# Performance work log

Measured on AMD Instinct MI355X. Metric: run time of the kernel, lower is better.

## Reference

```python
import jax, jax.numpy as jnp
import numpy as np

B, S, D = 4, 1024, 2048
H = 4096
NE = 8
TOPK = 2


def setup_inputs() -> dict:
    key = jax.random.key(0)
    ks = jax.random.split(key, 9)
    s = lambda fan_in: 1.0 / np.sqrt(fan_in)
    return {
        "x": jax.random.normal(ks[0], (B, S, D), dtype=jnp.float32),
        "W1": jax.random.normal(ks[1], (NE, D, H), dtype=jnp.float32) * s(D),
        "b1": jnp.zeros((NE, H), dtype=jnp.float32),
        "W2": jax.random.normal(ks[2], (NE, H, H), dtype=jnp.float32) * s(H),
        "b2": jnp.zeros((NE, H), dtype=jnp.float32),
        "W3": jax.random.normal(ks[3], (NE, H, D), dtype=jnp.float32) * s(H),
        "b3": jnp.zeros((NE, D), dtype=jnp.float32),
        "Wg": jax.random.normal(ks[4], (D, NE), dtype=jnp.float32) * s(D),
        "bg": jnp.zeros((NE,), dtype=jnp.float32),
    }


def reference(x, W1, b1, W2, b2, W3, b3, Wg, bg):
    # Gating: softmax over experts, then top-k
    gate_logits = jnp.einsum("bsd,dn->bsn", x, Wg) + bg          # [B,S,NE]
    gate_weights = jax.nn.softmax(gate_logits, axis=-1)
    topv, topi = jax.lax.top_k(gate_weights, TOPK)               # [B,S,K]

    # Dense compute of ALL experts (faithful to original)
    h = jax.nn.gelu(jnp.einsum("bsd,ndh->nbsh", x, W1) + b1[:, None, None, :], approximate=False)
    h = jax.nn.gelu(jnp.einsum("nbsh,nhf->nbsf", h, W2) + b2[:, None, None, :], approximate=False)
    eo = jnp.einsum("nbsf,nfd->nbsd", h, W3) + b3[:, None, None, :]  # [NE,B,S,D]

    # Weighted combine of top-k experts per token via sparse one-hot weights
    comb = jnp.sum(jax.nn.one_hot(topi, NE, dtype=x.dtype) * topv[..., None], axis=-2)  # [B,S,NE]
    out = jnp.einsum("nbsd,bsn->bsd", eo, comb)
    return out
```

## Files before the change

kernel.cpp:

```cpp
#include <hip/hip_runtime.h>
#include <math.h>

#define NT 4096
#define Dm 2048
#define Hm 4096
#define NEx 8
#define CAPROWS 9216

typedef float f32x4 __attribute__((ext_vector_type(4)));
typedef _Float16 f16x8 __attribute__((ext_vector_type(8)));

__global__ void k_init(int* meta) {
    if (threadIdx.x < NEx) meta[threadIdx.x] = 0;
}

__device__ __forceinline__ void conv_tile(const float* __restrict__ src, _Float16* __restrict__ dst,
                                          int K, int N, int t, float (*tile)[65]) {
    int nx = N >> 6, nk = K >> 6;
    int nb = t % nx;
    int kb = (t / nx) % nk;
    int e  = t / (nx * nk);
    int n0 = nb * 64, k0 = kb * 64;
    size_t ebase = (size_t)e * (size_t)K * (size_t)N;
    const float* S = src + ebase;
    _Float16* Dd = dst + ebase;
    int tx = threadIdx.x & 15, ty = threadIdx.x >> 4;
#pragma unroll
    for (int p = 0; p < 4; ++p) {
        int kr = p * 16 + ty;
        f32x4 v = *(const f32x4*)(S + (size_t)(k0 + kr) * N + n0 + tx * 4);
        tile[kr][tx * 4 + 0] = v[0]; tile[kr][tx * 4 + 1] = v[1];
        tile[kr][tx * 4 + 2] = v[2]; tile[kr][tx * 4 + 3] = v[3];
    }
    __syncthreads();
    int n = threadIdx.x >> 2, seg = threadIdx.x & 3;
    f16x8 o0, o1;
#pragma unroll
    for (int j = 0; j < 8; ++j) o0[j] = (_Float16)tile[seg * 16 + j][n];
#pragma unroll
    for (int j = 0; j < 8; ++j) o1[j] = (_Float16)tile[seg * 16 + 8 + j][n];
    _Float16* dp = Dd + (size_t)(n0 + n) * K + k0 + seg * 16;
    *(f16x8*)dp = o0;
    *(f16x8*)(dp + 8) = o1;
}

__global__ __launch_bounds__(256, 2) void k_convw(const float* __restrict__ src,
                                                  _Float16* __restrict__ dst, int K, int N) {
    __shared__ float tile[64][65];
    conv_tile(src, dst, K, N, blockIdx.x, tile);
}

__global__ __launch_bounds__(256, 2)
void k_gateconv(const float* __restrict__ x, const float* __restrict__ Wg,
                const float* __restrict__ bg, int* __restrict__ meta,
                int* __restrict__ list, float* __restrict__ topw,
                const float* __restrict__ csrc, _Float16* __restrict__ cdst,
                int cK, int cN) {
    __shared__ float tile[64][65];
    const int bid = blockIdx.x;
    if (bid >= NT / 4) {
        conv_tile(csrc, cdst, cK, cN, bid - NT / 4, tile);
        return;
    }
    int lane = threadIdx.x & 63;
    int t = bid * 4 + (threadIdx.x >> 6);
    const float* xr = x + (size_t)t * Dm;
    double acc[NEx];
#pragma unroll
    for (int j = 0; j < NEx; ++j) acc[j] = 0.0;
    for (int d = lane; d < Dm; d += 64) {
        double xv = (double)xr[d];
        const float* wr = Wg + (size_t)d * NEx;
#pragma unroll
        for (int j = 0; j < NEx; ++j) acc[j] += xv * (double)wr[j];
    }
#pragma unroll
    for (int off = 32; off > 0; off >>= 1) {
#pragma unroll
        for (int j = 0; j < NEx; ++j) acc[j] += __shfl_xor(acc[j], off, 64);
    }
    if (lane == 0) {
        double l[NEx];
#pragma unroll
        for (int j = 0; j < NEx; ++j) l[j] = acc[j] + (double)bg[j];
        double m = l[0];
        for (int j = 1; j < NEx; ++j) m = l[j] > m ? l[j] : m;
        double s = 0.0, ev[NEx];
        for (int j = 0; j < NEx; ++j) { ev[j] = exp(l[j] - m); s += ev[j]; }
        int i0 = 0; double v0 = l[0];
        for (int j = 1; j < NEx; ++j) if (l[j] > v0) { v0 = l[j]; i0 = j; }
        int i1 = -1; double v1 = -1e300;
        for (int j = 0; j < NEx; ++j) if (j != i0 && l[j] > v1) { v1 = l[j]; i1 = j; }
        topw[2 * t]     = (float)(ev[i0] / s);
        topw[2 * t + 1] = (float)(ev[i1] / s);
        int p0 = atomicAdd(&meta[i0], 1); list[i0 * NT + p0] = 2 * t;
        int p1 = atomicAdd(&meta[i1], 1); list[i1 * NT + p1] = 2 * t + 1;
    }
}

__global__ void k_plan(int* meta) {
    if (threadIdx.x == 0 && blockIdx.x == 0) {
        int tot = 0;
        for (int e = 0; e < NEx; ++e) {
            int c = meta[e];
            meta[8 + e] = c;
            int cp = (c + 127) & ~127;
            meta[16 + e] = cp;
            meta[24 + e] = tot;
            tot += cp;
        }
        meta[32] = tot;
    }
}

__global__ void k_gather(const float* __restrict__ x, const int* __restrict__ meta,
                         const int* __restrict__ list, int* __restrict__ pos_of,
                         _Float16* __restrict__ Xg) {
    int r = blockIdx.x;
    if (r >= meta[32]) return;
    int e = 0;
    while (r >= meta[24 + e + 1]) ++e;
    int i = r - meta[24 + e];
    _Float16* dst = Xg + (size_t)r * Dm + threadIdx.x * 8;
    if (i < meta[8 + e]) {
        int v = list[e * NT + i];
        int t = v >> 1;
        if (threadIdx.x == 0) pos_of[v] = r;
        const float* src = x + (size_t)t * Dm + threadIdx.x * 8;
        f32x4 a = *(const f32x4*)(src);
        f32x4 b = *(const f32x4*)(src + 4);
        f16x8 o;
        o[0] = (_Float16)a[0]; o[1] = (_Float16)a[1]; o[2] = (_Float16)a[2]; o[3] = (_Float16)a[3];
        o[4] = (_Float16)b[0]; o[5] = (_Float16)b[1]; o[6] = (_Float16)b[2]; o[7] = (_Float16)b[3];
        *(f16x8*)dst = o;
    } else {
        f16x8 z = (f16x8)(_Float16)0.0f;
        *(f16x8*)dst = z;
    }
}

__device__ __forceinline__ void gload16(const void* g, void* l) {
    __builtin_amdgcn_global_load_lds((__attribute__((address_space(1))) void*)(g),
                                     (__attribute__((address_space(3))) void*)(l),
                                     16, 0, 0);
}

__device__ __forceinline__ float gelu_f(float v) {
    return 0.5f * v * (1.0f + erff(v * 0.70710678118654752f));
}

template <int KDIM, int NDIM, bool GELU>
__global__ __launch_bounds__(256, 4)
void k_gemmconv(const _Float16* __restrict__ Abase, const _Float16* __restrict__ Wt,
                const float* __restrict__ bias, void* __restrict__ Cout,
                const int* __restrict__ meta,
                const float* __restrict__ csrc, _Float16* __restrict__ cdst,
                int cK, int cN, int nGemm) {
    __shared__ char smem[32768];
    const int bid = blockIdx.x;
    if (bid >= nGemm) {
        conv_tile(csrc, cdst, cK, cN, bid - nGemm, (float(*)[65])smem);
        return;
    }

    constexpr int GX = NDIM / 128;
    constexpr int GY = 32;
    constexpr int NBLK = GX * GY;
    const int e = bid / NBLK;
    const int f = bid % NBLK;
    const int fp = (f & 7) * (NBLK >> 3) + (f >> 3);
    const int nt = fp / GY;
    const int mt = fp % GY;
    const int cp = meta[16 + e];
    if (mt * 128 >= cp) return;
    const int row0 = meta[24 + e] + mt * 128;

    _Float16* ldsA = (_Float16*)smem;
    _Float16* ldsB = (_Float16*)(smem + 16384);

    const int tid = threadIdx.x;
    const int lane = tid & 63;
    const int wv = tid >> 6;
    const int wm = wv >> 1, wn = wv & 1;

    const char* Ag = (const char*)(Abase + (size_t)row0 * KDIM);
    const char* Bg = (const char*)(Wt + ((size_t)e * NDIM + (size_t)nt * 128) * KDIM);

    int soff[4];
#pragma unroll
    for (int r = 0; r < 4; ++r) {
        int L = r * 4096 + tid * 16;
        int row = L >> 7;
        int col = L & 127;
        int scol = col ^ ((row & 7) << 4);
        soff[r] = row * (KDIM * 2) + scol;
    }

    f32x4 acc[4][4];
#pragma unroll
    for (int i = 0; i < 4; ++i)
#pragma unroll
        for (int j = 0; j < 4; ++j)
            acc[i][j] = (f32x4){0.f, 0.f, 0.f, 0.f};

    int abase[4], aswz[4], bbase[4], bswz[4];
#pragma unroll
    for (int m = 0; m < 4; ++m) {
        int rA = wm * 64 + m * 16 + (lane & 15);
        abase[m] = rA * 128;
        aswz[m] = (rA & 7) << 4;
    }
#pragma unroll
    for (int n = 0; n < 4; ++n) {
        int rB = wn * 64 + n * 16 + (lane & 15);
        bbase[n] = rB * 128;
        bswz[n] = (rB & 7) << 4;
    }
    const int hib = (lane >> 4) * 16;

    const char* cldsA = (const char*)ldsA;
    const char* cldsB = (const char*)ldsB;

    for (int kt = 0; kt < KDIM / 64; ++kt) {
        const int kbyte = kt * 128;
#pragma unroll
        for (int r = 0; r < 4; ++r) {
            gload16(Ag + (soff[r] + kbyte), (char*)ldsA + r * 4096 + tid * 16);
            gload16(Bg + (soff[r] + kbyte), (char*)ldsB + r * 4096 + tid * 16);
        }
        __syncthreads();
#pragma unroll
        for (int ks = 0; ks < 2; ++ks) {
            const int cbs = ks * 64 + hib;
            f16x8 av[4], bv[4];
#pragma unroll
            for (int m = 0; m < 4; ++m)
                av[m] = *(const f16x8*)(cldsA + abase[m] + (cbs ^ aswz[m]));
#pragma unroll
            for (int n = 0; n < 4; ++n)
                bv[n] = *(const f16x8*)(cldsB + bbase[n] + (cbs ^ bswz[n]));
#pragma unroll
            for (int m = 0; m < 4; ++m)
#pragma unroll
                for (int n = 0; n < 4; ++n)
                    acc[m][n] = __builtin_amdgcn_mfma_f32_16x16x32_f16(av[m], bv[n], acc[m][n], 0, 0, 0);
        }
        __syncthreads();
    }

    const int lcol = lane & 15;
    const int rowq = (lane >> 4) * 4;
#pragma unroll
    for (int m = 0; m < 4; ++m) {
#pragma unroll
        for (int n = 0; n < 4; ++n) {
            const int gcol = nt * 128 + wn * 64 + n * 16 + lcol;
            const float bb = bias[(size_t)e * NDIM + gcol];
#pragma unroll
            for (int v = 0; v < 4; ++v) {
                const int grow = row0 + wm * 64 + m * 16 + rowq + v;
                float val = acc[m][n][v] + bb;
                if constexpr (GELU) {
                    ((_Float16*)Cout)[(size_t)grow * NDIM + gcol] = (_Float16)gelu_f(val);
                } else {
                    ((float*)Cout)[(size_t)grow * NDIM + gcol] = val;
                }
            }
        }
    }
}

__global__ void k_combine(const float* __restrict__ eo, const int* __restrict__ pos_of,
                          const float* __restrict__ topw, float* __restrict__ out) {
    int t = blockIdx.x;
    int r0 = pos_of[2 * t], r1 = pos_of[2 * t + 1];
    float w0 = topw[2 * t], w1 = topw[2 * t + 1];
    const f32x4* e0 = (const f32x4*)(eo + (size_t)r0 * Dm);
    const f32x4* e1 = (const f32x4*)(eo + (size_t)r1 * Dm);
    f32x4* op = (f32x4*)(out + (size_t)t * Dm);
    for (int i = threadIdx.x; i < Dm / 4; i += 256) {
        f32x4 a = e0[i], b = e1[i];
        op[i] = a * w0 + b * w1;
    }
}

extern "C" void kernel_launch(void* const* d_in, const int* in_sizes, int n_in,
                              void* d_out, int out_size, void* d_ws, size_t ws_size,
                              hipStream_t stream) {
    const float* x  = (const float*)d_in[0];
    const float* W1 = (const float*)d_in[1];
    const float* b1 = (const float*)d_in[2];
    const float* W2 = (const float*)d_in[3];
    const float* b2 = (const float*)d_in[4];
    const float* W3 = (const float*)d_in[5];
    const float* b3 = (const float*)d_in[6];
    const float* Wg = (const float*)d_in[7];
    const float* bg = (const float*)d_in[8];
    float* out = (float*)d_out;
    (void)in_sizes; (void)n_in; (void)out_size;

    char* ws = (char*)d_ws;
    int*   meta   = (int*)ws;
    int*   list   = (int*)(ws + 256);
    int*   pos_of = (int*)(ws + 256 + 131072);
    float* topw   = (float*)(ws + 256 + 131072 + 32768);
    size_t off = 196864;

    const int nC1 = (Hm / 64) * (Dm / 64) * NEx;
    const int nC2 = (Hm / 64) * (Hm / 64) * NEx;
    const int nC3 = (Dm / 64) * (Hm / 64) * NEx;
    const int nG12 = NEx * (Hm / 128) * 32;
    const int nG3  = NEx * (Dm / 128) * 32;

    const size_t sXg  = (size_t)CAPROWS * Dm * 2;
    const size_t sWb1 = (size_t)NEx * Dm * Hm * 2;
    const size_t sWb2 = (size_t)NEx * Hm * Hm * 2;
    const size_t sWb3 = (size_t)NEx * Hm * Dm * 2;
    const size_t sH   = (size_t)CAPROWS * Hm * 2;

    const size_t needPar = off + sXg + sWb1 + sWb2 + sWb3 + sH + sH;

    if (ws_size >= needPar) {
        _Float16* Xg  = (_Float16*)(ws + off); off += sXg;
        _Float16* Wb1 = (_Float16*)(ws + off); off += sWb1;
        _Float16* Wb2 = (_Float16*)(ws + off); off += sWb2;
        _Float16* Wb3 = (_Float16*)(ws + off); off += sWb3;
        _Float16* h1  = (_Float16*)(ws + off); off += sH;
        _Float16* h2  = (_Float16*)(ws + off); off += sH;
        float*    eo  = (float*)Wb1;

        k_init<<<1, 64, 0, stream>>>(meta);
        k_gateconv<<<NT / 4 + nC1, 256, 0, stream>>>(x, Wg, bg, meta, list, topw,
                                                     W1, Wb1, Dm, Hm);
        k_plan<<<1, 1, 0, stream>>>(meta);
        k_gather<<<CAPROWS, 256, 0, stream>>>(x, meta, list, pos_of, Xg);

        k_gemmconv<Dm, Hm, true><<<nG12 + nC2, 256, 0, stream>>>(
            Xg, Wb1, b1, (void*)h1, meta, W2, Wb2, Hm, Hm, nG12);
        k_gemmconv<Hm, Hm, true><<<nG12 + nC3, 256, 0, stream>>>(
            h1, Wb2, b2, (void*)h2, meta, W3, Wb3, Hm, Dm, nG12);
        k_gemmconv<Hm, Dm, false><<<nG3, 256, 0, stream>>>(
            h2, Wb3, b3, (void*)eo, meta, (const float*)0, (_Float16*)0, 0, 0, nG3);

        k_combine<<<NT, 256, 0, stream>>>(eo, pos_of, topw, out);
    } else {
        _Float16* Xg = (_Float16*)(ws + off); off += sXg;
        _Float16* Wb = (_Float16*)(ws + off); off += sWb2;
        _Float16* h2 = (_Float16*)(ws + off); off += sH;
        _Float16* h1 = (_Float16*)(ws + off);
        float*    eo = (float*)(ws + off);

        k_init<<<1, 64, 0, stream>>>(meta);
        k_gateconv<<<NT / 4, 256, 0, stream>>>(x, Wg, bg, meta, list, topw,
                                               (const float*)0, (_Float16*)0, 0, 0);
        k_plan<<<1, 1, 0, stream>>>(meta);
        k_gather<<<CAPROWS, 256, 0, stream>>>(x, meta, list, pos_of, Xg);

        k_convw<<<nC1, 256, 0, stream>>>(W1, Wb, Dm, Hm);
        k_gemmconv<Dm, Hm, true><<<nG12, 256, 0, stream>>>(
            Xg, Wb, b1, (void*)h1, meta, (const float*)0, (_Float16*)0, 0, 0, nG12);

        k_convw<<<nC2, 256, 0, stream>>>(W2, Wb, Hm, Hm);
        k_gemmconv<Hm, Hm, true><<<nG12, 256, 0, stream>>>(
            h1, Wb, b2, (void*)h2, meta, (const float*)0, (_Float16*)0, 0, 0, nG12);

        k_convw<<<nC3, 256, 0, stream>>>(W3, Wb, Hm, Dm);
        k_gemmconv<Hm, Dm, false><<<nG3, 256, 0, stream>>>(
            h2, Wb, b3, (void*)eo, meta, (const float*)0, (_Float16*)0, 0, 0, nG3);

        k_combine<<<NT, 256, 0, stream>>>(eo, pos_of, topw, out);
    }
}
```

Measured before the change: 1.098 ms.

## Fuse top-k combine into final expert GEMM epilogue via atomic adds

The final expert GEMM now scales each output row by its gate weight and atomically accumulates it into the output token row, using per-row token and weight tables written during gather. This removes the separate combine kernel and the fp32 expert-output round trip through memory. A memset of the output is added. The weight conversion tiles also switch to nontemporal loads and stores so streamed weights pollute the cache less. Atomic float adds make the summation order nondeterministic and add atomic traffic.

```diff
diff --git a/kernel.cpp b/kernel.cpp
--- a/kernel.cpp
+++ b/kernel.cpp
@@ -28,7 +28,7 @@
 #pragma unroll
     for (int p = 0; p < 4; ++p) {
         int kr = p * 16 + ty;
-        f32x4 v = *(const f32x4*)(S + (size_t)(k0 + kr) * N + n0 + tx * 4);
+        f32x4 v = __builtin_nontemporal_load((const f32x4*)(S + (size_t)(k0 + kr) * N + n0 + tx * 4));
         tile[kr][tx * 4 + 0] = v[0]; tile[kr][tx * 4 + 1] = v[1];
         tile[kr][tx * 4 + 2] = v[2]; tile[kr][tx * 4 + 3] = v[3];
     }
@@ -40,8 +40,8 @@
 #pragma unroll
     for (int j = 0; j < 8; ++j) o1[j] = (_Float16)tile[seg * 16 + 8 + j][n];
     _Float16* dp = Dd + (size_t)(n0 + n) * K + k0 + seg * 16;
-    *(f16x8*)dp = o0;
-    *(f16x8*)(dp + 8) = o1;
+    __builtin_nontemporal_store(o0, (f16x8*)dp);
+    __builtin_nontemporal_store(o1, (f16x8*)(dp + 8));
 }
 
 __global__ __launch_bounds__(256, 2) void k_convw(const float* __restrict__ src,
@@ -114,7 +114,8 @@
 }
 
 __global__ void k_gather(const float* __restrict__ x, const int* __restrict__ meta,
-                         const int* __restrict__ list, int* __restrict__ pos_of,
+                         const int* __restrict__ list, const float* __restrict__ topw,
+                         int* __restrict__ tok_of, float* __restrict__ wsc,
                          _Float16* __restrict__ Xg) {
     int r = blockIdx.x;
     if (r >= meta[32]) return;
@@ -125,7 +126,7 @@
     if (i < meta[8 + e]) {
         int v = list[e * NT + i];
         int t = v >> 1;
-        if (threadIdx.x == 0) pos_of[v] = r;
+        if (threadIdx.x == 0) { tok_of[r] = t; wsc[r] = topw[v]; }
         const float* src = x + (size_t)t * Dm + threadIdx.x * 8;
         f32x4 a = *(const f32x4*)(src);
         f32x4 b = *(const f32x4*)(src + 4);
@@ -134,6 +135,7 @@
         o[4] = (_Float16)b[0]; o[5] = (_Float16)b[1]; o[6] = (_Float16)b[2]; o[7] = (_Float16)b[3];
         *(f16x8*)dst = o;
     } else {
+        if (threadIdx.x == 0) { tok_of[r] = -1; wsc[r] = 0.0f; }
         f16x8 z = (f16x8)(_Float16)0.0f;
         *(f16x8*)dst = z;
     }
@@ -149,11 +151,13 @@
     return 0.5f * v * (1.0f + erff(v * 0.70710678118654752f));
 }
 
-template <int KDIM, int NDIM, bool GELU>
+template <int KDIM, int NDIM, bool GELU, bool FC>
 __global__ __launch_bounds__(256, 4)
 void k_gemmconv(const _Float16* __restrict__ Abase, const _Float16* __restrict__ Wt,
                 const float* __restrict__ bias, void* __restrict__ Cout,
                 const int* __restrict__ meta,
+                const int* __restrict__ tok_of, const float* __restrict__ wsc,
+                float* __restrict__ outp,
                 const float* __restrict__ csrc, _Float16* __restrict__ cdst,
                 int cK, int cN, int nGemm) {
     __shared__ char smem[32768];
@@ -250,37 +254,47 @@
 
     const int lcol = lane & 15;
     const int rowq = (lane >> 4) * 4;
-#pragma unroll
-    for (int m = 0; m < 4; ++m) {
-#pragma unroll
-        for (int n = 0; n < 4; ++n) {
-            const int gcol = nt * 128 + wn * 64 + n * 16 + lcol;
-            const float bb = bias[(size_t)e * NDIM + gcol];
+    if constexpr (FC) {
+        float bb[4];
+#pragma unroll
+        for (int n = 0; n < 4; ++n)
+            bb[n] = bias[(size_t)e * NDIM + nt * 128 + wn * 64 + n * 16 + lcol];
+#pragma unroll
+        for (int m = 0; m < 4; ++m) {
 #pragma unroll
             for (int v = 0; v < 4; ++v) {
                 const int grow = row0 + wm * 64 + m * 16 + rowq + v;
-                float val = acc[m][n][v] + bb;
-                if constexpr (GELU) {
-                    ((_Float16*)Cout)[(size_t)grow * NDIM + gcol] = (_Float16)gelu_f(val);
-                } else {
-                    ((float*)Cout)[(size_t)grow * NDIM + gcol] = val;
+                const int tok = tok_of[grow];
+                if (tok >= 0) {
+                    const float w = wsc[grow];
+                    float* orow = outp + (size_t)tok * NDIM;
+#pragma unroll
+                    for (int n = 0; n < 4; ++n) {
+                        const int gcol = nt * 128 + wn * 64 + n * 16 + lcol;
+                        atomicAdd(orow + gcol, w * (acc[m][n][v] + bb[n]));
+                    }
                 }
             }
         }
-    }
-}
-
-__global__ void k_combine(const float* __restrict__ eo, const int* __restrict__ pos_of,
-                          const float* __restrict__ topw, float* __restrict__ out) {
-    int t = blockIdx.x;
-    int r0 = pos_of[2 * t], r1 = pos_of[2 * t + 1];
-    float w0 = topw[2 * t], w1 = topw[2 * t + 1];
-    const f32x4* e0 = (const f32x4*)(eo + (size_t)r0 * Dm);
-    const f32x4* e1 = (const f32x4*)(eo + (size_t)r1 * Dm);
-    f32x4* op = (f32x4*)(out + (size_t)t * Dm);
-    for (int i = threadIdx.x; i < Dm / 4; i += 256) {
-        f32x4 a = e0[i], b = e1[i];
-        op[i] = a * w0 + b * w1;
+    } else {
+#pragma unroll
+        for (int m = 0; m < 4; ++m) {
+#pragma unroll
+            for (int n = 0; n < 4; ++n) {
+                const int gcol = nt * 128 + wn * 64 + n * 16 + lcol;
+                const float bb = bias[(size_t)e * NDIM + gcol];
+#pragma unroll
+                for (int v = 0; v < 4; ++v) {
+                    const int grow = row0 + wm * 64 + m * 16 + rowq + v;
+                    float val = acc[m][n][v] + bb;
+                    if constexpr (GELU) {
+                        ((_Float16*)Cout)[(size_t)grow * NDIM + gcol] = (_Float16)gelu_f(val);
+                    } else {
+                        ((float*)Cout)[(size_t)grow * NDIM + gcol] = val;
+                    }
+                }
+            }
+        }
     }
 }
 
@@ -297,14 +311,15 @@
     const float* Wg = (const float*)d_in[7];
     const float* bg = (const float*)d_in[8];
     float* out = (float*)d_out;
-    (void)in_sizes; (void)n_in; (void)out_size;
+    (void)in_sizes; (void)n_in;
 
     char* ws = (char*)d_ws;
     int*   meta   = (int*)ws;
     int*   list   = (int*)(ws + 256);
-    int*   pos_of = (int*)(ws + 256 + 131072);
-    float* topw   = (float*)(ws + 256 + 131072 + 32768);
-    size_t off = 196864;
+    int*   tok_of = (int*)(ws + 256 + 131072);
+    float* wsc    = (float*)(ws + 256 + 131072 + 36864);
+    float* topw   = (float*)(ws + 256 + 131072 + 73728);
+    size_t off = 237824;
 
     const int nC1 = (Hm / 64) * (Dm / 64) * NEx;
     const int nC2 = (Hm / 64) * (Hm / 64) * NEx;
@@ -319,6 +334,8 @@
     const size_t sH   = (size_t)CAPROWS * Hm * 2;
 
     const size_t needPar = off + sXg + sWb1 + sWb2 + sWb3 + sH + sH;
+
+    hipMemsetAsync(out, 0, (size_t)out_size * sizeof(float), stream);
 
     if (ws_size >= needPar) {
         _Float16* Xg  = (_Float16*)(ws + off); off += sXg;
@@ -327,47 +344,47 @@
         _Float16* Wb3 = (_Float16*)(ws + off); off += sWb3;
         _Float16* h1  = (_Float16*)(ws + off); off += sH;
         _Float16* h2  = (_Float16*)(ws + off); off += sH;
-        float*    eo  = (float*)Wb1;
 
         k_init<<<1, 64, 0, stream>>>(meta);
         k_gateconv<<<NT / 4 + nC1, 256, 0, stream>>>(x, Wg, bg, meta, list, topw,
                                                      W1, Wb1, Dm, Hm);
         k_plan<<<1, 1, 0, stream>>>(meta);
-        k_gather<<<CAPROWS, 256, 0, stream>>>(x, meta, list, pos_of, Xg);
-
-        k_gemmconv<Dm, Hm, true><<<nG12 + nC2, 256, 0, stream>>>(
-            Xg, Wb1, b1, (void*)h1, meta, W2, Wb2, Hm, Hm, nG12);
-        k_gemmconv<Hm, Hm, true><<<nG12 + nC3, 256, 0, stream>>>(
-            h1, Wb2, b2, (void*)h2, meta, W3, Wb3, Hm, Dm, nG12);
-        k_gemmconv<Hm, Dm, false><<<nG3, 256, 0, stream>>>(
-            h2, Wb3, b3, (void*)eo, meta, (const float*)0, (_Float16*)0, 0, 0, nG3);
-
-        k_combine<<<NT, 256, 0, stream>>>(eo, pos_of, topw, out);
+        k_gather<<<CAPROWS, 256, 0, stream>>>(x, meta, list, topw, tok_of, wsc, Xg);
+
+        k_gemmconv<Dm, Hm, true, false><<<nG12 + nC2, 256, 0, stream>>>(
+            Xg, Wb1, b1, (void*)h1, meta, (const int*)0, (const float*)0, (float*)0,
+            W2, Wb2, Hm, Hm, nG12);
+        k_gemmconv<Hm, Hm, true, false><<<nG12 + nC3, 256, 0, stream>>>(
+            h1, Wb2, b2, (void*)h2, meta, (const int*)0, (const float*)0, (float*)0,
+            W3, Wb3, Hm, Dm, nG12);
+        k_gemmconv<Hm, Dm, false, true><<<nG3, 256, 0, stream>>>(
+            h2, Wb3, b3, (void*)0, meta, tok_of, wsc, out,
+            (const float*)0, (_Float16*)0, 0, 0, nG3);
     } else {
         _Float16* Xg = (_Float16*)(ws + off); off += sXg;
         _Float16* Wb = (_Float16*)(ws + off); off += sWb2;
         _Float16* h2 = (_Float16*)(ws + off); off += sH;
         _Float16* h1 = (_Float16*)(ws + off);
-        float*    eo = (float*)(ws + off);
 
         k_init<<<1, 64, 0, stream>>>(meta);
         k_gateconv<<<NT / 4, 256, 0, stream>>>(x, Wg, bg, meta, list, topw,
                                                (const float*)0, (_Float16*)0, 0, 0);
         k_plan<<<1, 1, 0, stream>>>(meta);
-        k_gather<<<CAPROWS, 256, 0, stream>>>(x, meta, list, pos_of, Xg);
+        k_gather<<<CAPROWS, 256, 0, stream>>>(x, meta, list, topw, tok_of, wsc, Xg);
 
         k_convw<<<nC1, 256, 0, stream>>>(W1, Wb, Dm, Hm);
-        k_gemmconv<Dm, Hm, true><<<nG12, 256, 0, stream>>>(
-            Xg, Wb, b1, (void*)h1, meta, (const float*)0, (_Float16*)0, 0, 0, nG12);
+        k_gemmconv<Dm, Hm, true, false><<<nG12, 256, 0, stream>>>(
+            Xg, Wb, b1, (void*)h1, meta, (const int*)0, (const float*)0, (float*)0,
+            (const float*)0, (_Float16*)0, 0, 0, nG12);
 
         k_convw<<<nC2, 256, 0, stream>>>(W2, Wb, Hm, Hm);
-        k_gemmconv<Hm, Hm, true><<<nG12, 256, 0, stream>>>(
-            h1, Wb, b2, (void*)h2, meta, (const float*)0, (_Float16*)0, 0, 0, nG12);
+        k_gemmconv<Hm, Hm, true, false><<<nG12, 256, 0, stream>>>(
+            h1, Wb, b2, (void*)h2, meta, (const int*)0, (const float*)0, (float*)0,
+            (const float*)0, (_Float16*)0, 0, 0, nG12);
 
         k_convw<<<nC3, 256, 0, stream>>>(W3, Wb, Hm, Dm);
-        k_gemmconv<Hm, Dm, false><<<nG3, 256, 0, stream>>>(
-            h2, Wb, b3, (void*)eo, meta, (const float*)0, (_Float16*)0, 0, 0, nG3);
-
-        k_combine<<<NT, 256, 0, stream>>>(eo, pos_of, topw, out);
-    }
-}
+        k_gemmconv<Hm, Dm, false, true><<<nG3, 256, 0, stream>>>(
+            h2, Wb, b3, (void*)0, meta, tok_of, wsc, out,
+            (const float*)0, (_Float16*)0, 0, 0, nG3);
+    }
+}
```

Result: no change. 1.113 ms (+1.4%).

## Make weight-conversion blocks persistent with prefetch and nontemporal accesses

Applied to the files above, without the earlier changes.

Replaces the one-tile-per-block fp32→fp16 weight transpose with persistent worker blocks that loop over tiles. Each worker prefetches the next tile into registers while it writes out the current one. Loads and stores become nontemporal so the streamed weights do not evict GEMM data from cache. Fewer conversion blocks are launched alongside the GEMM blocks, which cuts block launch overhead and changes how conversion work shares the GPU with the concurrent GEMM tiles.

```diff
diff --git a/kernel.cpp b/kernel.cpp
--- a/kernel.cpp
+++ b/kernel.cpp
@@ -14,40 +14,61 @@
     if (threadIdx.x < NEx) meta[threadIdx.x] = 0;
 }
 
-__device__ __forceinline__ void conv_tile(const float* __restrict__ src, _Float16* __restrict__ dst,
-                                          int K, int N, int t, float (*tile)[65]) {
-    int nx = N >> 6, nk = K >> 6;
-    int nb = t % nx;
-    int kb = (t / nx) % nk;
-    int e  = t / (nx * nk);
-    int n0 = nb * 64, k0 = kb * 64;
-    size_t ebase = (size_t)e * (size_t)K * (size_t)N;
-    const float* S = src + ebase;
-    _Float16* Dd = dst + ebase;
-    int tx = threadIdx.x & 15, ty = threadIdx.x >> 4;
-#pragma unroll
-    for (int p = 0; p < 4; ++p) {
-        int kr = p * 16 + ty;
-        f32x4 v = *(const f32x4*)(S + (size_t)(k0 + kr) * N + n0 + tx * 4);
-        tile[kr][tx * 4 + 0] = v[0]; tile[kr][tx * 4 + 1] = v[1];
-        tile[kr][tx * 4 + 2] = v[2]; tile[kr][tx * 4 + 3] = v[3];
-    }
-    __syncthreads();
-    int n = threadIdx.x >> 2, seg = threadIdx.x & 3;
-    f16x8 o0, o1;
-#pragma unroll
-    for (int j = 0; j < 8; ++j) o0[j] = (_Float16)tile[seg * 16 + j][n];
-#pragma unroll
-    for (int j = 0; j < 8; ++j) o1[j] = (_Float16)tile[seg * 16 + 8 + j][n];
-    _Float16* dp = Dd + (size_t)(n0 + n) * K + k0 + seg * 16;
-    *(f16x8*)dp = o0;
-    *(f16x8*)(dp + 8) = o1;
+__device__ void conv_worker(const float* __restrict__ src, _Float16* __restrict__ dst,
+                            int K, int N, int total, int wid, int nw,
+                            float (*tile)[65]) {
+    const int tx = threadIdx.x & 15, ty = threadIdx.x >> 4;
+    const int nx = N >> 6, nk = K >> 6;
+    int t = wid;
+    if (t >= total) return;
+
+    auto loadt = [&](int tt, f32x4* vv) {
+        int nb = tt % nx; int kb = (tt / nx) % nk; int e = tt / (nx * nk);
+        const float* S = src + (size_t)e * K * N + (size_t)(kb * 64) * N + nb * 64;
+#pragma unroll
+        for (int p = 0; p < 4; ++p)
+            vv[p] = __builtin_nontemporal_load(
+                (const f32x4*)(S + (size_t)(p * 16 + ty) * N + tx * 4));
+    };
+
+    f32x4 v[4];
+    loadt(t, v);
+    for (;;) {
+#pragma unroll
+        for (int p = 0; p < 4; ++p) {
+            int kr = p * 16 + ty;
+            tile[kr][tx * 4 + 0] = v[p][0]; tile[kr][tx * 4 + 1] = v[p][1];
+            tile[kr][tx * 4 + 2] = v[p][2]; tile[kr][tx * 4 + 3] = v[p][3];
+        }
+        __syncthreads();
+        const int tn = t + nw;
+        f32x4 v2[4];
+        if (tn < total) loadt(tn, v2);
+        const int n = threadIdx.x >> 2, seg = threadIdx.x & 3;
+        f16x8 o0, o1;
+#pragma unroll
+        for (int j = 0; j < 8; ++j) o0[j] = (_Float16)tile[seg * 16 + j][n];
+#pragma unroll
+        for (int j = 0; j < 8; ++j) o1[j] = (_Float16)tile[seg * 16 + 8 + j][n];
+        {
+            int nb = t % nx; int kb = (t / nx) % nk; int e = t / (nx * nk);
+            _Float16* dp = dst + (size_t)e * K * N + (size_t)(nb * 64 + n) * K + kb * 64 + seg * 16;
+            __builtin_nontemporal_store(o0, (f16x8*)dp);
+            __builtin_nontemporal_store(o1, (f16x8*)(dp + 8));
+        }
+        if (tn >= total) return;
+        __syncthreads();
+#pragma unroll
+        for (int p = 0; p < 4; ++p) v[p] = v2[p];
+        t = tn;
+    }
 }
 
 __global__ __launch_bounds__(256, 2) void k_convw(const float* __restrict__ src,
-                                                  _Float16* __restrict__ dst, int K, int N) {
+                                                  _Float16* __restrict__ dst, int K, int N,
+                                                  int total) {
     __shared__ float tile[64][65];
-    conv_tile(src, dst, K, N, blockIdx.x, tile);
+    conv_worker(src, dst, K, N, total, blockIdx.x, gridDim.x, tile);
 }
 
 __global__ __launch_bounds__(256, 2)
@@ -55,11 +76,11 @@
                 const float* __restrict__ bg, int* __restrict__ meta,
                 int* __restrict__ list, float* __restrict__ topw,
                 const float* __restrict__ csrc, _Float16* __restrict__ cdst,
-                int cK, int cN) {
+                int cK, int cN, int cTotal) {
     __shared__ float tile[64][65];
     const int bid = blockIdx.x;
     if (bid >= NT / 4) {
-        conv_tile(csrc, cdst, cK, cN, bid - NT / 4, tile);
+        conv_worker(csrc, cdst, cK, cN, cTotal, bid - NT / 4, gridDim.x - NT / 4, tile);
         return;
     }
     int lane = threadIdx.x & 63;
@@ -155,11 +176,13 @@
                 const float* __restrict__ bias, void* __restrict__ Cout,
                 const int* __restrict__ meta,
                 const float* __restrict__ csrc, _Float16* __restrict__ cdst,
-                int cK, int cN, int nGemm) {
+                int cK, int cN, int cTotal,
+                int nGemm) {
     __shared__ char smem[32768];
     const int bid = blockIdx.x;
     if (bid >= nGemm) {
-        conv_tile(csrc, cdst, cK, cN, bid - nGemm, (float(*)[65])smem);
+        conv_worker(csrc, cdst, cK, cN, cTotal, bid - nGemm, gridDim.x - nGemm,
+                    (float(*)[65])smem);
         return;
     }
 
@@ -309,6 +332,7 @@
     const int nC1 = (Hm / 64) * (Dm / 64) * NEx;
     const int nC2 = (Hm / 64) * (Hm / 64) * NEx;
     const int nC3 = (Dm / 64) * (Hm / 64) * NEx;
+    const int CW1 = 2048, CW2 = 2048, CW3 = 1024;
     const int nG12 = NEx * (Hm / 128) * 32;
     const int nG3  = NEx * (Dm / 128) * 32;
 
@@ -330,17 +354,18 @@
         float*    eo  = (float*)Wb1;
 
         k_init<<<1, 64, 0, stream>>>(meta);
-        k_gateconv<<<NT / 4 + nC1, 256, 0, stream>>>(x, Wg, bg, meta, list, topw,
-                                                     W1, Wb1, Dm, Hm);
+        k_gateconv<<<NT / 4 + CW1, 256, 0, stream>>>(x, Wg, bg, meta, list, topw,
+                                                     W1, Wb1, Dm, Hm, nC1);
         k_plan<<<1, 1, 0, stream>>>(meta);
         k_gather<<<CAPROWS, 256, 0, stream>>>(x, meta, list, pos_of, Xg);
 
-        k_gemmconv<Dm, Hm, true><<<nG12 + nC2, 256, 0, stream>>>(
-            Xg, Wb1, b1, (void*)h1, meta, W2, Wb2, Hm, Hm, nG12);
-        k_gemmconv<Hm, Hm, true><<<nG12 + nC3, 256, 0, stream>>>(
-            h1, Wb2, b2, (void*)h2, meta, W3, Wb3, Hm, Dm, nG12);
+        k_gemmconv<Dm, Hm, true><<<nG12 + CW2, 256, 0, stream>>>(
+            Xg, Wb1, b1, (void*)h1, meta, W2, Wb2, Hm, Hm, nC2, nG12);
+        k_gemmconv<Hm, Hm, true><<<nG12 + CW3, 256, 0, stream>>>(
+            h1, Wb2, b2, (void*)h2, meta, W3, Wb3, Hm, Dm, nC3, nG12);
         k_gemmconv<Hm, Dm, false><<<nG3, 256, 0, stream>>>(
-            h2, Wb3, b3, (void*)eo, meta, (const float*)0, (_Float16*)0, 0, 0, nG3);
+            h2, Wb3, b3, (void*)eo, meta,
+            (const float*)0, (_Float16*)0, 0, 0, 0, nG3);
 
         k_combine<<<NT, 256, 0, stream>>>(eo, pos_of, topw, out);
     } else {
@@ -352,21 +377,24 @@
 
         k_init<<<1, 64, 0, stream>>>(meta);
         k_gateconv<<<NT / 4, 256, 0, stream>>>(x, Wg, bg, meta, list, topw,
-                                               (const float*)0, (_Float16*)0, 0, 0);
+                                               (const float*)0, (_Float16*)0, 0, 0, 0);
         k_plan<<<1, 1, 0, stream>>>(meta);
         k_gather<<<CAPROWS, 256, 0, stream>>>(x, meta, list, pos_of, Xg);
 
-        k_convw<<<nC1, 256, 0, stream>>>(W1, Wb, Dm, Hm);
+        k_convw<<<CW1, 256, 0, stream>>>(W1, Wb, Dm, Hm, nC1);
         k_gemmconv<Dm, Hm, true><<<nG12, 256, 0, stream>>>(
-            Xg, Wb, b1, (void*)h1, meta, (const float*)0, (_Float16*)0, 0, 0, nG12);
-
-        k_convw<<<nC2, 256, 0, stream>>>(W2, Wb, Hm, Hm);
+            Xg, Wb, b1, (void*)h1, meta,
+            (const float*)0, (_Float16*)0, 0, 0, 0, nG12);
+
+        k_convw<<<CW2, 256, 0, stream>>>(W2, Wb, Hm, Hm, nC2);
         k_gemmconv<Hm, Hm, true><<<nG12, 256, 0, stream>>>(
-            h1, Wb, b2, (void*)h2, meta, (const float*)0, (_Float16*)0, 0, 0, nG12);
-
-        k_convw<<<nC3, 256, 0, stream>>>(W3, Wb, Hm, Dm);
+            h1, Wb, b2, (void*)h2, meta,
+            (const float*)0, (_Float16*)0, 0, 0, 0, nG12);
+
+        k_convw<<<CW3, 256, 0, stream>>>(W3, Wb, Hm, Dm, nC3);
         k_gemmconv<Hm, Dm, false><<<nG3, 256, 0, stream>>>(
-            h2, Wb, b3, (void*)eo, meta, (const float*)0, (_Float16*)0, 0, 0, nG3);
+            h2, Wb, b3, (void*)eo, meta,
+            (const float*)0, (_Float16*)0, 0, 0, 0, nG3);
 
         k_combine<<<NT, 256, 0, stream>>>(eo, pos_of, topw, out);
     }
```

Measured after the change: 1.173 ms. +6.9%, slower.
